# Kernel tuning notes

Hardware: AMD Instinct MI355X
Metric: run time of the kernel (lower is better)

## Reference

```python
import jax, jax.numpy as jnp
import numpy as np

B, T, DM, H = 4, 2048, 1024, 16
D = DM // H  # head_dim = 64


def setup_inputs() -> dict:
    key = jax.random.key(0)
    ks = jax.random.split(key, 10)
    s = 0.02
    return {
        "query": jax.random.normal(ks[0], (B, T, DM), jnp.float32),
        "key": jax.random.normal(ks[1], (B, T, DM), jnp.float32),
        "value": jax.random.normal(ks[2], (B, T, DM), jnp.float32),
        "Wq": jax.random.normal(ks[3], (DM, DM), jnp.float32) * s,
        "bq": jnp.zeros((DM,), jnp.float32),
        "Wk": jax.random.normal(ks[4], (DM, DM), jnp.float32) * s,
        "bk": jnp.zeros((DM,), jnp.float32),
        "Wv": jax.random.normal(ks[5], (DM, DM), jnp.float32) * s,
        "bv": jnp.zeros((DM,), jnp.float32),
        "Wo": jax.random.normal(ks[6], (DM, DM), jnp.float32) * s,
        "bo": jnp.zeros((DM,), jnp.float32),
        "gate_w": jax.random.normal(ks[7], (H, D, D), jnp.float32) * s,
        "gate_b": jax.random.normal(ks[8], (H, D), jnp.float32),
    }


def _split_heads(x):
    # (B, T, DM) -> (B, H, T, D)
    b, t, _ = x.shape
    return x.reshape(b, t, H, D).transpose(0, 2, 1, 3)


def reference(query, key, value, Wq, bq, Wk, bk, Wv, bv, Wo, bo, gate_w, gate_b):
    q = _split_heads(query @ Wq + bq)   # (B,H,T,D)
    k = _split_heads(key @ Wk + bk)
    v = _split_heads(value @ Wv + bv)
    scale = 1.0 / jnp.sqrt(jnp.asarray(D, q.dtype))
    scores = jnp.einsum("bhqd,bhkd->bhqk", q, k) * scale  # (B,H,Tq,Tk)
    attn = jax.nn.softmax(scores, axis=-1)
    y = jnp.einsum("bhqk,bhkd->bhqd", attn, v)            # (B,H,T,D)
    # per-head elementwise gating: sigmoid(W_h y + b_h)
    gate = jax.nn.sigmoid(jnp.einsum("bhtd,hde->bhte", y, gate_w) + gate_b[None, :, None, :])
    y = y * gate
    y = y.transpose(0, 2, 1, 3).reshape(y.shape[0], y.shape[2], H * D)  # merge heads
    return y @ Wo + bo
```

## Files before the change

kernel.cpp:

```cpp
#include <hip/hip_runtime.h>
#include <stdint.h>

typedef unsigned short u16;
typedef uint32_t u32;
typedef __attribute__((ext_vector_type(8))) short bf16x8;
typedef __attribute__((ext_vector_type(4))) float f32x4;
typedef __attribute__((ext_vector_type(4))) u32 u32x4;

__device__ __forceinline__ u16 f2b(float x) {
  union { float f; uint32_t u; } v; v.f = x;
  uint32_t u = v.u;
  return (u16)((u + 0x7fffu + ((u >> 16) & 1u)) >> 16);
}

__device__ __forceinline__ float fexp2(float x) {
  float r;
  asm("v_exp_f32 %0, %1" : "=v"(r) : "v"(x));
  return r;
}

__device__ __forceinline__ u32 cvtpk(float lo, float hi) {
  u32 r;
  asm("v_cvt_pk_bf16_f32 %0, %1, %2" : "=v"(r) : "v"(lo), "v"(hi));
  return r;
}

__device__ __forceinline__ void gload_lds16(const void* g, void* l) {
  __builtin_amdgcn_global_load_lds(
      (const __attribute__((address_space(1))) void*)g,
      (__attribute__((address_space(3))) void*)l, 16, 0, 0);
}

__global__ __launch_bounds__(256) void cvt3_f32_bf16(const float* __restrict__ q,
                                                     const float* __restrict__ k,
                                                     const float* __restrict__ v,
                                                     u16* __restrict__ xq,
                                                     u16* __restrict__ xk,
                                                     u16* __restrict__ xv, int n4) {
  int idx = blockIdx.x * 256 + threadIdx.x;
  if (idx >= n4) return;
  const int z = blockIdx.y;
  const float* in = z == 0 ? q : z == 1 ? k : v;
  u16* out = z == 0 ? xq : z == 1 ? xk : xv;
  float4 vv = ((const float4*)in)[idx];
  ushort4 o;
  o.x = f2b(vv.x); o.y = f2b(vv.y); o.z = f2b(vv.z); o.w = f2b(vv.w);
  ((ushort4*)out)[idx] = o;
}

__global__ __launch_bounds__(256) void transpose_cvt4(const float* __restrict__ w0,
                                                      const float* __restrict__ w1,
                                                      const float* __restrict__ w2,
                                                      const float* __restrict__ w3,
                                                      u16* __restrict__ o0,
                                                      u16* __restrict__ o1,
                                                      u16* __restrict__ o2,
                                                      u16* __restrict__ o3) {
  __shared__ float t[64][65];
  const int z = blockIdx.z;
  const float* inp = z == 0 ? w0 : z == 1 ? w1 : z == 2 ? w2 : w3;
  u16* outp = z == 0 ? o0 : z == 1 ? o1 : z == 2 ? o2 : o3;
  int r0 = blockIdx.x * 64, c0 = blockIdx.y * 64;
  for (int i = 0; i < 16; ++i) {
    int idx = i * 256 + threadIdx.x;
    int r = idx >> 6, c = idx & 63;
    t[r][c] = inp[(size_t)(r0 + r) * 1024 + (c0 + c)];
  }
  __syncthreads();
  for (int i = 0; i < 16; ++i) {
    int idx = i * 256 + threadIdx.x;
    int c = idx >> 6, r = idx & 63;
    outp[(size_t)(c0 + c) * 1024 + (r0 + r)] = f2b(t[r][c]);
  }
}

__global__ __launch_bounds__(256) void transpose_gate(const float* __restrict__ in,
                                                      u16* __restrict__ out) {
  __shared__ float t[64][65];
  const float* inp = in + (size_t)blockIdx.z * 4096;
  u16* outp = out + (size_t)blockIdx.z * 4096;
  for (int i = 0; i < 16; ++i) {
    int idx = i * 256 + threadIdx.x;
    int r = idx >> 6, c = idx & 63;
    t[r][c] = inp[(size_t)r * 64 + c];
  }
  __syncthreads();
  for (int i = 0; i < 16; ++i) {
    int idx = i * 256 + threadIdx.x;
    int c = idx >> 6, r = idx & 63;
    outp[(size_t)c * 64 + r] = f2b(t[r][c]);
  }
}

template <int MODE>
__device__ __forceinline__ void gemm_body(const u16* __restrict__ A,
                                          const u16* __restrict__ Bt,
                                          const float* __restrict__ bias,
                                          void* __restrict__ Cout,
                                          int M, int N, int K, float scale,
                                          u16* lA, u16* lB, int bm, int bn) {
  const int tid = threadIdx.x;
  const int wave = tid >> 6, lane = tid & 63;
  const int l15 = lane & 15, l4 = lane >> 4;
  const int wr = (wave >> 1) * 64, wc = (wave & 1) * 64;
  f32x4 acc[4][4];
  for (int a = 0; a < 4; ++a)
    for (int b = 0; b < 4; ++b)
      for (int j = 0; j < 4; ++j) acc[a][b][j] = 0.f;
  const u16* Ab = A + (size_t)bm * 128 * K;
  const u16* Bb = Bt + (size_t)bn * 128 * K;
  for (int kt = 0; kt < K; kt += 64) {
    __syncthreads();
#pragma unroll
    for (int i = 0; i < 4; ++i) {
      int p = i * 256 + tid;
      int r = p >> 3, kc = p & 7, skc = kc ^ (r & 7);
      gload_lds16(Ab + (size_t)r * K + kt + skc * 8, &lA[p * 8]);
    }
#pragma unroll
    for (int i = 0; i < 4; ++i) {
      int p = i * 256 + tid;
      int r = p >> 3, kc = p & 7, skc = kc ^ (r & 7);
      gload_lds16(Bb + (size_t)r * K + kt + skc * 8, &lB[p * 8]);
    }
    __syncthreads();
#pragma unroll
    for (int kk = 0; kk < 2; ++kk) {
      const int kch = kk * 4 + l4;
      bf16x8 af[4], bfr[4];
#pragma unroll
      for (int mt = 0; mt < 4; ++mt) {
        int r = wr + mt * 16 + l15;
        af[mt] = *(const bf16x8*)&lA[r * 64 + ((kch ^ (r & 7)) << 3)];
      }
#pragma unroll
      for (int nt = 0; nt < 4; ++nt) {
        int r = wc + nt * 16 + l15;
        bfr[nt] = *(const bf16x8*)&lB[r * 64 + ((kch ^ (r & 7)) << 3)];
      }
      __builtin_amdgcn_s_setprio(1);
#pragma unroll
      for (int mt = 0; mt < 4; ++mt)
#pragma unroll
        for (int nt = 0; nt < 4; ++nt)
          acc[mt][nt] = __builtin_amdgcn_mfma_f32_16x16x32_bf16(af[mt], bfr[nt],
                                                                acc[mt][nt], 0, 0, 0);
      __builtin_amdgcn_s_setprio(0);
    }
  }
  float bval[4];
  float bvalm[4][4];
  if constexpr (MODE == 2) {
#pragma unroll
    for (int mt = 0; mt < 4; ++mt)
#pragma unroll
      for (int i = 0; i < 4; ++i)
        bvalm[mt][i] = bias[bm * 128 + wr + mt * 16 + l4 * 4 + i];
  } else {
#pragma unroll
    for (int nt = 0; nt < 4; ++nt) bval[nt] = bias[bn * 128 + wc + nt * 16 + l15];
  }
#pragma unroll
  for (int mt = 0; mt < 4; ++mt) {
#pragma unroll
    for (int nt = 0; nt < 4; ++nt) {
      int n = bn * 128 + wc + nt * 16 + l15;
#pragma unroll
      for (int i = 0; i < 4; ++i) {
        int m = bm * 128 + wr + mt * 16 + l4 * 4 + i;
        if constexpr (MODE == 0) {
          ((float*)Cout)[(size_t)m * N + n] = acc[mt][nt][i] + bval[nt];
        } else if constexpr (MODE == 1) {
          float v = acc[mt][nt][i] + bval[nt];
          int bb = m >> 11, t = m & 2047, hh = n >> 6, d = n & 63;
          ((u16*)Cout)[(((size_t)bb * 16 + hh) * 2048 + t) * 64 + d] = f2b(v * scale);
        } else {
          float v = acc[mt][nt][i] + bvalm[mt][i];
          int bb = n >> 11, t = n & 2047, hh = m >> 6, d = m & 63;
          ((u16*)Cout)[(((size_t)bb * 16 + hh) * 64 + d) * 2048 + t] = f2b(v);
        }
      }
    }
  }
}

__device__ __forceinline__ void gemm_swizzle(int& i64, int& i8) {
  int lid = blockIdx.x + (blockIdx.y << 6);
  int xcd = lid & 7, s = lid >> 3;
  i64 = xcd * 8 + (s & 7);
  i8 = s >> 3;
}

__global__ __launch_bounds__(256) void gemm_qkv(const u16* __restrict__ Xq,
                                                const u16* __restrict__ Xk,
                                                const u16* __restrict__ Xv,
                                                const u16* __restrict__ WqT,
                                                const u16* __restrict__ WkT,
                                                const u16* __restrict__ WvT,
                                                const float* __restrict__ bq,
                                                const float* __restrict__ bk,
                                                const float* __restrict__ bv,
                                                u16* __restrict__ Qb,
                                                u16* __restrict__ Kb,
                                                u16* __restrict__ Vtr, float qscale) {
  __shared__ __align__(16) u16 lA[128 * 64];
  __shared__ __align__(16) u16 lB[128 * 64];
  const int z = blockIdx.z;
  int i64, i8;
  gemm_swizzle(i64, i8);
  if (z == 2) {
    gemm_body<2>(WvT, Xv, bv, Vtr, 1024, 8192, 1024, 1.0f, lA, lB, i8, i64);
  } else {
    const u16* A = z == 0 ? Xq : Xk;
    const u16* Bt = z == 0 ? WqT : WkT;
    const float* bias = z == 0 ? bq : bk;
    u16* C = z == 0 ? Qb : Kb;
    float scale = z == 0 ? qscale : 1.0f;
    gemm_body<1>(A, Bt, bias, C, 8192, 1024, 1024, scale, lA, lB, i64, i8);
  }
}

__global__ __launch_bounds__(256) void gemm_out(const u16* __restrict__ A,
                                                const u16* __restrict__ Bt,
                                                const float* __restrict__ bias,
                                                float* __restrict__ C) {
  __shared__ __align__(16) u16 lA[128 * 64];
  __shared__ __align__(16) u16 lB[128 * 64];
  int i64, i8;
  gemm_swizzle(i64, i8);
  gemm_body<0>(A, Bt, bias, C, 8192, 1024, 1024, 1.0f, lA, lB, i64, i8);
}

__global__ __launch_bounds__(256) void attn_fused(const u16* __restrict__ Qb,
                                                  const u16* __restrict__ Kb,
                                                  const u16* __restrict__ Vt,
                                                  const u16* __restrict__ GwT,
                                                  const float* __restrict__ gate_b,
                                                  u16* __restrict__ Yg) {
  __shared__ __align__(16) u16 lds[16384];
  const int tid = threadIdx.x;
  const int w = tid >> 6, lane = tid & 63;
  const int l15 = lane & 15, l4 = lane >> 4;
  const int bid = blockIdx.x;
  const int xcd = bid & 7, slot = bid >> 3;
  const int bh = xcd * 8 + (slot >> 4);
  const int qt = slot & 15;
  const int b = bh >> 4, h = bh & 15;

  const u16* QgA = Qb + ((size_t)bh * 2048 + qt * 128 + w * 32 + l15) * 64;
  const u16* QgB = QgA + 16 * 64;
  bf16x8 qA0 = *(const bf16x8*)(QgA + l4 * 8);
  bf16x8 qA1 = *(const bf16x8*)(QgA + 32 + l4 * 8);
  bf16x8 qB0 = *(const bf16x8*)(QgB + l4 * 8);
  bf16x8 qB1 = *(const bf16x8*)(QgB + 32 + l4 * 8);

  const bf16x8 ones = {0x3F80, 0x3F80, 0x3F80, 0x3F80, 0x3F80, 0x3F80, 0x3F80, 0x3F80};
  const f32x4 fz = {0.f, 0.f, 0.f, 0.f};

  f32x4 accA[4], accB[4], lsA, lsB;
#pragma unroll
  for (int nt = 0; nt < 4; ++nt)
#pragma unroll
    for (int j = 0; j < 4; ++j) { accA[nt][j] = 0.f; accB[nt][j] = 0.f; }
#pragma unroll
  for (int j = 0; j < 4; ++j) { lsA[j] = 0.f; lsB[j] = 0.f; }

  const u16* f0 = lds + l15 * 64 + ((l4 ^ (l15 & 7)) << 3);
  const u16* f1 = lds + l15 * 64 + (((4 + l4) ^ (l15 & 7)) << 3);

  const int r0 = tid >> 3, kc0 = tid & 7, skc = kc0 ^ (r0 & 7);
  const int sr = ((r0 << 1) & 0x38) | ((r0 >> 3) & 4) | (r0 & 3);
  const u16* kp  = Kb + (size_t)bh * 131072 + (size_t)sr * 64 + skc * 8;
  const u16* kp2 = kp + 256;
  const u16* vp  = Vt + (size_t)bh * 131072 + (size_t)r0 * 2048 + skc * 8;
  const u16* vp2 = vp + (size_t)32 * 2048;
  u16* dK = lds + tid * 8;
  u16* dV = lds + 8192 + tid * 8;

#define STAGE(c)                                                     \
  do {                                                               \
    gload_lds16(kp, dK + (c)*4096);                                  \
    gload_lds16(kp2, dK + (c)*4096 + 2048);                          \
    gload_lds16(vp, dV + (c)*4096);                                  \
    gload_lds16(vp2, dV + (c)*4096 + 2048);                          \
    kp += 4096; kp2 += 4096; vp += 64; vp2 += 64;                    \
  } while (0)

#define COMPUTE(c)                                                            \
  do {                                                                        \
    bf16x8 kf0[4], kf1[4];                                                    \
    _Pragma("unroll") for (int nt = 0; nt < 4; ++nt) {                        \
      kf0[nt] = *(const bf16x8*)(f0 + (c)*4096 + nt * 1024);                  \
      kf1[nt] = *(const bf16x8*)(f1 + (c)*4096 + nt * 1024);                  \
    }                                                                         \
    f32x4 sA[4], sB[4];                                                       \
    __builtin_amdgcn_s_setprio(1);                                            \
    _Pragma("unroll") for (int nt = 0; nt < 4; ++nt) {                        \
      sA[nt] = __builtin_amdgcn_mfma_f32_16x16x32_bf16(kf0[nt], qA0, fz, 0, 0, 0); \
      sA[nt] = __builtin_amdgcn_mfma_f32_16x16x32_bf16(kf1[nt], qA1, sA[nt], 0, 0, 0); \
      sB[nt] = __builtin_amdgcn_mfma_f32_16x16x32_bf16(kf0[nt], qB0, fz, 0, 0, 0); \
      sB[nt] = __builtin_amdgcn_mfma_f32_16x16x32_bf16(kf1[nt], qB1, sB[nt], 0, 0, 0); \
    }                                                                         \
    __builtin_amdgcn_s_setprio(0);                                            \
    union { u32x4 u; bf16x8 bv; } a0, a1, b0, b1;                             \
    a0.u[0] = cvtpk(fexp2(sA[0][0]), fexp2(sA[0][1]));                        \
    a0.u[1] = cvtpk(fexp2(sA[0][2]), fexp2(sA[0][3]));                        \
    a0.u[2] = cvtpk(fexp2(sA[2][0]), fexp2(sA[2][1]));                        \
    a0.u[3] = cvtpk(fexp2(sA[2][2]), fexp2(sA[2][3]));                        \
    a1.u[0] = cvtpk(fexp2(sA[1][0]), fexp2(sA[1][1]));                        \
    a1.u[1] = cvtpk(fexp2(sA[1][2]), fexp2(sA[1][3]));                        \
    a1.u[2] = cvtpk(fexp2(sA[3][0]), fexp2(sA[3][1]));                        \
    a1.u[3] = cvtpk(fexp2(sA[3][2]), fexp2(sA[3][3]));                        \
    b0.u[0] = cvtpk(fexp2(sB[0][0]), fexp2(sB[0][1]));                        \
    b0.u[1] = cvtpk(fexp2(sB[0][2]), fexp2(sB[0][3]));                        \
    b0.u[2] = cvtpk(fexp2(sB[2][0]), fexp2(sB[2][1]));                        \
    b0.u[3] = cvtpk(fexp2(sB[2][2]), fexp2(sB[2][3]));                        \
    b1.u[0] = cvtpk(fexp2(sB[1][0]), fexp2(sB[1][1]));                        \
    b1.u[1] = cvtpk(fexp2(sB[1][2]), fexp2(sB[1][3]));                        \
    b1.u[2] = cvtpk(fexp2(sB[3][0]), fexp2(sB[3][1]));                        \
    b1.u[3] = cvtpk(fexp2(sB[3][2]), fexp2(sB[3][3]));                        \
    __builtin_amdgcn_s_setprio(1);                                            \
    lsA = __builtin_amdgcn_mfma_f32_16x16x32_bf16(ones, a0.bv, lsA, 0, 0, 0); \
    lsA = __builtin_amdgcn_mfma_f32_16x16x32_bf16(ones, a1.bv, lsA, 0, 0, 0); \
    lsB = __builtin_amdgcn_mfma_f32_16x16x32_bf16(ones, b0.bv, lsB, 0, 0, 0); \
    lsB = __builtin_amdgcn_mfma_f32_16x16x32_bf16(ones, b1.bv, lsB, 0, 0, 0); \
    bf16x8 vf0[4], vf1[4];                                                    \
    _Pragma("unroll") for (int nt = 0; nt < 4; ++nt) {                        \
      vf0[nt] = *(const bf16x8*)(f0 + 8192 + (c)*4096 + nt * 1024);           \
      vf1[nt] = *(const bf16x8*)(f1 + 8192 + (c)*4096 + nt * 1024);           \
    }                                                                         \
    _Pragma("unroll") for (int nt = 0; nt < 4; ++nt) {                        \
      accA[nt] = __builtin_amdgcn_mfma_f32_16x16x32_bf16(vf0[nt], a0.bv, accA[nt], 0, 0, 0); \
      accA[nt] = __builtin_amdgcn_mfma_f32_16x16x32_bf16(vf1[nt], a1.bv, accA[nt], 0, 0, 0); \
      accB[nt] = __builtin_amdgcn_mfma_f32_16x16x32_bf16(vf0[nt], b0.bv, accB[nt], 0, 0, 0); \
      accB[nt] = __builtin_amdgcn_mfma_f32_16x16x32_bf16(vf1[nt], b1.bv, accB[nt], 0, 0, 0); \
    }                                                                         \
    __builtin_amdgcn_s_setprio(0);                                            \
  } while (0)

  STAGE(0);
  __syncthreads();
  for (int it = 0; it < 16; ++it) {
    STAGE(1);
    COMPUTE(0);
    __syncthreads();
    if (it < 15) STAGE(0);
    COMPUTE(1);
    __syncthreads();
  }
#undef STAGE
#undef COMPUTE

  bf16x8 gwf[2][4];
  {
    const u16* g = GwT + (size_t)h * 4096;
#pragma unroll
    for (int kk = 0; kk < 2; ++kk)
#pragma unroll
      for (int et = 0; et < 4; ++et)
        gwf[kk][et] = *(const bf16x8*)(g + (et * 16 + l15) * 64 + (kk * 4 + l4) * 8);
  }
  const float* gb = gate_b + h * 64;
  const int rsw = (l15 & 7) << 2;

#define EPILOGUE(accX, lsX, g)                                                 \
  do {                                                                         \
    float inv = 1.f / lsX[0];                                                  \
    float y[4][4];                                                             \
    _Pragma("unroll") for (int nt = 0; nt < 4; ++nt)                           \
      _Pragma("unroll") for (int i = 0; i < 4; ++i) y[nt][i] = accX[nt][i] * inv; \
    u32* ws32 = (u32*)lds + w * 2048 + (g)*1024;                               \
    _Pragma("unroll") for (int nt = 0; nt < 4; ++nt) {                         \
      u32 y0 = cvtpk(y[nt][0], y[nt][1]);                                      \
      u32 y1 = cvtpk(y[nt][2], y[nt][3]);                                      \
      int col = (nt * 8 + l4 * 2) ^ rsw;                                       \
      *(uint64_t*)(ws32 + l15 * 64 + col) = ((uint64_t)y1 << 32) | y0;         \
    }                                                                          \
    asm volatile("s_waitcnt lgkmcnt(0)" ::: "memory");                         \
    bf16x8 yf[2];                                                              \
    yf[0] = *(const bf16x8*)(ws32 + l15 * 64 + ((l4 * 4) ^ rsw));              \
    yf[1] = *(const bf16x8*)(ws32 + l15 * 64 + ((16 + l4 * 4) ^ rsw));         \
    f32x4 g4[4];                                                               \
    _Pragma("unroll") for (int et = 0; et < 4; ++et)                           \
      _Pragma("unroll") for (int j = 0; j < 4; ++j) g4[et][j] = 0.f;           \
    _Pragma("unroll") for (int kk = 0; kk < 2; ++kk)                           \
      _Pragma("unroll") for (int et = 0; et < 4; ++et)                         \
        g4[et] = __builtin_amdgcn_mfma_f32_16x16x32_bf16(gwf[kk][et], yf[kk], g4[et], 0, 0, 0); \
    u32 ok[4][2];                                                              \
    _Pragma("unroll") for (int et = 0; et < 4; ++et) {                         \
      float o[4];                                                              \
      _Pragma("unroll") for (int i = 0; i < 4; ++i) {                          \
        float gv = g4[et][i] + gb[et * 16 + l4 * 4 + i];                       \
        float sg = 1.f / (1.f + __expf(-gv));                                  \
        o[i] = y[et][i] * sg;                                                  \
      }                                                                        \
      ok[et][0] = cvtpk(o[0], o[1]);                                           \
      ok[et][1] = cvtpk(o[2], o[3]);                                           \
    }                                                                          \
    asm volatile("s_waitcnt lgkmcnt(0)" ::: "memory");                         \
    _Pragma("unroll") for (int et = 0; et < 4; ++et) {                         \
      int col = (et * 8 + l4 * 2) ^ rsw;                                       \
      *(uint64_t*)(ws32 + l15 * 64 + col) = ((uint64_t)ok[et][1] << 32) | ok[et][0]; \
    }                                                                          \
    asm volatile("s_waitcnt lgkmcnt(0)" ::: "memory");                         \
    {                                                                          \
      int rr = lane >> 2, c = lane & 3;                                        \
      int rs2 = (rr & 7) << 2;                                                 \
      u32x4 d0 = *(const u32x4*)(ws32 + rr * 64 + ((c * 4) ^ rs2));            \
      u32x4 d1 = *(const u32x4*)(ws32 + rr * 64 + (((c + 4) * 4) ^ rs2));      \
      size_t row = (size_t)b * 2048 + qt * 128 + w * 32 + (g)*16 + rr;         \
      u32* og = (u32*)(Yg + row * 1024 + h * 64);                              \
      *(u32x4*)(og + c * 4) = d0;                                              \
      *(u32x4*)(og + (c + 4) * 4) = d1;                                        \
    }                                                                          \
  } while (0)

  EPILOGUE(accA, lsA, 0);
  EPILOGUE(accB, lsB, 1);
#undef EPILOGUE
}

extern "C" void kernel_launch(void* const* d_in, const int* in_sizes, int n_in,
                              void* d_out, int out_size, void* d_ws, size_t ws_size,
                              hipStream_t stream) {
  (void)in_sizes; (void)n_in; (void)out_size; (void)ws_size;
  const float* query  = (const float*)d_in[0];
  const float* key    = (const float*)d_in[1];
  const float* value  = (const float*)d_in[2];
  const float* Wq     = (const float*)d_in[3];
  const float* bq     = (const float*)d_in[4];
  const float* Wk     = (const float*)d_in[5];
  const float* bk     = (const float*)d_in[6];
  const float* Wv     = (const float*)d_in[7];
  const float* bv     = (const float*)d_in[8];
  const float* Wo     = (const float*)d_in[9];
  const float* bo     = (const float*)d_in[10];
  const float* gate_w = (const float*)d_in[11];
  const float* gate_b = (const float*)d_in[12];

  const size_t XN = (size_t)8192 * 1024;
  const size_t WN = (size_t)1024 * 1024;
  char* ws = (char*)d_ws;
  size_t off = 0;
  auto nxt = [&](size_t bytes) {
    char* p = ws + off;
    off += (bytes + 255) & ~(size_t)255;
    return p;
  };
  u16* Xq  = (u16*)nxt(XN * 2);
  u16* Xk  = (u16*)nxt(XN * 2);
  u16* Xv  = (u16*)nxt(XN * 2);
  u16* WqT = (u16*)nxt(WN * 2);
  u16* WkT = (u16*)nxt(WN * 2);
  u16* WvT = (u16*)nxt(WN * 2);
  u16* WoT = (u16*)nxt(WN * 2);
  u16* GwT = (u16*)nxt((size_t)16 * 64 * 64 * 2);
  u16* Qb  = (u16*)nxt(XN * 2);
  u16* Kb  = (u16*)nxt(XN * 2);
  u16* Vtr = (u16*)nxt(XN * 2);
  u16* Yg  = (u16*)nxt(XN * 2);

  int n4 = (int)(XN / 4);
  cvt3_f32_bf16<<<dim3(n4 / 256, 3), 256, 0, stream>>>(query, key, value, Xq, Xk, Xv, n4);
  transpose_cvt4<<<dim3(16, 16, 4), 256, 0, stream>>>(Wq, Wk, Wv, Wo, WqT, WkT, WvT, WoT);
  transpose_gate<<<dim3(1, 1, 16), 256, 0, stream>>>(gate_w, GwT);

  gemm_qkv<<<dim3(64, 8, 3), 256, 0, stream>>>(Xq, Xk, Xv, WqT, WkT, WvT, bq, bk, bv,
                                               Qb, Kb, Vtr, 0.125f * 1.44269504f);
  attn_fused<<<1024, 256, 0, stream>>>(Qb, Kb, Vtr, GwT, gate_b, Yg);
  gemm_out<<<dim3(64, 8), 256, 0, stream>>>(Yg, WoT, bo, (float*)d_out);
}
```

Before: 206.7 us.

## Software-pipeline attention loop with triple-buffered K/V and skewed QK/PV stages

The fused attention loop is restructured into a three-stage software pipeline. The exp/convert work for one KV chunk overlaps the PV MFMAs of the previous chunk and the QK^T MFMAs of the next chunk, and K/V staging in LDS moves from two buffers to three. The aim is to hide the transcendental latency and the global-to-LDS loads behind matrix work, replacing __syncthreads with an explicit vmcnt wait plus barrier. In exchange it uses more LDS (48 KB) and keeps score and probability registers live across stages, which may cut occupancy.

```diff
diff --git a/kernel.cpp b/kernel.cpp
--- a/kernel.cpp
+++ b/kernel.cpp
@@ -237,7 +237,7 @@
                                                   const u16* __restrict__ GwT,
                                                   const float* __restrict__ gate_b,
                                                   u16* __restrict__ Yg) {
-  __shared__ __align__(16) u16 lds[16384];
+  __shared__ __align__(16) u16 lds[24576];
   const int tid = threadIdx.x;
   const int w = tid >> 6, lane = tid & 63;
   const int l15 = lane & 15, l4 = lane >> 4;
@@ -265,6 +265,9 @@
 #pragma unroll
   for (int j = 0; j < 4; ++j) { lsA[j] = 0.f; lsB[j] = 0.f; }
 
+  f32x4 sA[4], sB[4];
+  bf16x8 pA0, pA1, pB0, pB1;
+
   const u16* f0 = lds + l15 * 64 + ((l4 ^ (l15 & 7)) << 3);
   const u16* f1 = lds + l15 * 64 + (((4 + l4) ^ (l15 & 7)) << 3);
 
@@ -275,7 +278,7 @@
   const u16* vp  = Vt + (size_t)bh * 131072 + (size_t)r0 * 2048 + skc * 8;
   const u16* vp2 = vp + (size_t)32 * 2048;
   u16* dK = lds + tid * 8;
-  u16* dV = lds + 8192 + tid * 8;
+  u16* dV = lds + 12288 + tid * 8;
 
 #define STAGE(c)                                                     \
   do {                                                               \
@@ -286,14 +289,13 @@
     kp += 4096; kp2 += 4096; vp += 64; vp2 += 64;                    \
   } while (0)
 
-#define COMPUTE(c)                                                            \
+#define QKT(c)                                                                \
   do {                                                                        \
     bf16x8 kf0[4], kf1[4];                                                    \
     _Pragma("unroll") for (int nt = 0; nt < 4; ++nt) {                        \
       kf0[nt] = *(const bf16x8*)(f0 + (c)*4096 + nt * 1024);                  \
       kf1[nt] = *(const bf16x8*)(f1 + (c)*4096 + nt * 1024);                  \
     }                                                                         \
-    f32x4 sA[4], sB[4];                                                       \
     __builtin_amdgcn_s_setprio(1);                                            \
     _Pragma("unroll") for (int nt = 0; nt < 4; ++nt) {                        \
       sA[nt] = __builtin_amdgcn_mfma_f32_16x16x32_bf16(kf0[nt], qA0, fz, 0, 0, 0); \
@@ -302,6 +304,10 @@
       sB[nt] = __builtin_amdgcn_mfma_f32_16x16x32_bf16(kf1[nt], qB1, sB[nt], 0, 0, 0); \
     }                                                                         \
     __builtin_amdgcn_s_setprio(0);                                            \
+  } while (0)
+
+#define EXPP()                                                                \
+  do {                                                                        \
     union { u32x4 u; bf16x8 bv; } a0, a1, b0, b1;                             \
     a0.u[0] = cvtpk(fexp2(sA[0][0]), fexp2(sA[0][1]));                        \
     a0.u[1] = cvtpk(fexp2(sA[0][2]), fexp2(sA[0][3]));                        \
@@ -319,37 +325,62 @@
     b1.u[1] = cvtpk(fexp2(sB[1][2]), fexp2(sB[1][3]));                        \
     b1.u[2] = cvtpk(fexp2(sB[3][0]), fexp2(sB[3][1]));                        \
     b1.u[3] = cvtpk(fexp2(sB[3][2]), fexp2(sB[3][3]));                        \
-    __builtin_amdgcn_s_setprio(1);                                            \
-    lsA = __builtin_amdgcn_mfma_f32_16x16x32_bf16(ones, a0.bv, lsA, 0, 0, 0); \
-    lsA = __builtin_amdgcn_mfma_f32_16x16x32_bf16(ones, a1.bv, lsA, 0, 0, 0); \
-    lsB = __builtin_amdgcn_mfma_f32_16x16x32_bf16(ones, b0.bv, lsB, 0, 0, 0); \
-    lsB = __builtin_amdgcn_mfma_f32_16x16x32_bf16(ones, b1.bv, lsB, 0, 0, 0); \
+    pA0 = a0.bv; pA1 = a1.bv; pB0 = b0.bv; pB1 = b1.bv;                       \
+  } while (0)
+
+#define PVC(c)                                                                \
+  do {                                                                        \
     bf16x8 vf0[4], vf1[4];                                                    \
     _Pragma("unroll") for (int nt = 0; nt < 4; ++nt) {                        \
-      vf0[nt] = *(const bf16x8*)(f0 + 8192 + (c)*4096 + nt * 1024);           \
-      vf1[nt] = *(const bf16x8*)(f1 + 8192 + (c)*4096 + nt * 1024);           \
+      vf0[nt] = *(const bf16x8*)(f0 + 12288 + (c)*4096 + nt * 1024);          \
+      vf1[nt] = *(const bf16x8*)(f1 + 12288 + (c)*4096 + nt * 1024);          \
     }                                                                         \
+    __builtin_amdgcn_s_setprio(1);                                            \
+    lsA = __builtin_amdgcn_mfma_f32_16x16x32_bf16(ones, pA0, lsA, 0, 0, 0);   \
+    lsA = __builtin_amdgcn_mfma_f32_16x16x32_bf16(ones, pA1, lsA, 0, 0, 0);   \
+    lsB = __builtin_amdgcn_mfma_f32_16x16x32_bf16(ones, pB0, lsB, 0, 0, 0);   \
+    lsB = __builtin_amdgcn_mfma_f32_16x16x32_bf16(ones, pB1, lsB, 0, 0, 0);   \
     _Pragma("unroll") for (int nt = 0; nt < 4; ++nt) {                        \
-      accA[nt] = __builtin_amdgcn_mfma_f32_16x16x32_bf16(vf0[nt], a0.bv, accA[nt], 0, 0, 0); \
-      accA[nt] = __builtin_amdgcn_mfma_f32_16x16x32_bf16(vf1[nt], a1.bv, accA[nt], 0, 0, 0); \
-      accB[nt] = __builtin_amdgcn_mfma_f32_16x16x32_bf16(vf0[nt], b0.bv, accB[nt], 0, 0, 0); \
-      accB[nt] = __builtin_amdgcn_mfma_f32_16x16x32_bf16(vf1[nt], b1.bv, accB[nt], 0, 0, 0); \
+      accA[nt] = __builtin_amdgcn_mfma_f32_16x16x32_bf16(vf0[nt], pA0, accA[nt], 0, 0, 0); \
+      accA[nt] = __builtin_amdgcn_mfma_f32_16x16x32_bf16(vf1[nt], pA1, accA[nt], 0, 0, 0); \
+      accB[nt] = __builtin_amdgcn_mfma_f32_16x16x32_bf16(vf0[nt], pB0, accB[nt], 0, 0, 0); \
+      accB[nt] = __builtin_amdgcn_mfma_f32_16x16x32_bf16(vf1[nt], pB1, accB[nt], 0, 0, 0); \
     }                                                                         \
     __builtin_amdgcn_s_setprio(0);                                            \
   } while (0)
 
+#define VBAR()                                        \
+  do {                                                \
+    asm volatile("s_waitcnt vmcnt(0)" ::: "memory");  \
+    __builtin_amdgcn_s_barrier();                     \
+  } while (0)
+
+#define ITER(cp, cn) \
+  do { STAGE(cn); PVC(cp); EXPP(); VBAR(); QKT(cn); } while (0)
+
   STAGE(0);
+  VBAR();
+  QKT(0);
+  STAGE(1);
+  EXPP();
+  VBAR();
+  QKT(1);
+
+  for (int it = 0; it < 10; ++it) {
+    ITER(0, 2);
+    ITER(1, 0);
+    ITER(2, 1);
+  }
+  PVC(0);
+  EXPP();
+  PVC(1);
   __syncthreads();
-  for (int it = 0; it < 16; ++it) {
-    STAGE(1);
-    COMPUTE(0);
-    __syncthreads();
-    if (it < 15) STAGE(0);
-    COMPUTE(1);
-    __syncthreads();
-  }
 #undef STAGE
-#undef COMPUTE
+#undef QKT
+#undef EXPP
+#undef PVC
+#undef VBAR
+#undef ITER
 
   bf16x8 gwf[2][4];
   {
```

After: 203.7 us. About the same (-1.4%).

## Use 256x128 GEMM tiles with 512 threads and triple-buffered async LDS loads

Applied to the files above, without the earlier changes.

Replaces the 128x128, 256-thread GEMM body with a 256x128 tile run by 8 waves. Global-to-LDS loads are triple-buffered so the next two K-steps are in flight during compute, with vmcnt waits and one barrier per step instead of two syncthreads. Source and fragment addresses are precomputed, and the block-to-tile mapping is changed to spread tiles across XCDs. The cost is 144KB of LDS per block and a grid that shrinks to 256 blocks per GEMM, which may limit occupancy.

```diff
diff --git a/kernel.cpp b/kernel.cpp
--- a/kernel.cpp
+++ b/kernel.cpp
@@ -93,61 +93,101 @@
 }
 
 template <int MODE>
-__device__ __forceinline__ void gemm_body(const u16* __restrict__ A,
-                                          const u16* __restrict__ Bt,
-                                          const float* __restrict__ bias,
-                                          void* __restrict__ Cout,
-                                          int M, int N, int K, float scale,
-                                          u16* lA, u16* lB, int bm, int bn) {
+__device__ __forceinline__ void gemm256_body(const u16* __restrict__ A,
+                                             const u16* __restrict__ Bt,
+                                             const float* __restrict__ bias,
+                                             void* __restrict__ Cout,
+                                             int M, int N, int K, float scale,
+                                             u16* lds, int bm, int bn) {
   const int tid = threadIdx.x;
-  const int wave = tid >> 6, lane = tid & 63;
+  const int w = tid >> 6, lane = tid & 63;
   const int l15 = lane & 15, l4 = lane >> 4;
-  const int wr = (wave >> 1) * 64, wc = (wave & 1) * 64;
+  const int wm = w & 3, wn = w >> 2;
+  const int wr = wm * 64, wc = wn * 64;
+
   f32x4 acc[4][4];
+#pragma unroll
   for (int a = 0; a < 4; ++a)
+#pragma unroll
     for (int b = 0; b < 4; ++b)
+#pragma unroll
       for (int j = 0; j < 4; ++j) acc[a][b][j] = 0.f;
-  const u16* Ab = A + (size_t)bm * 128 * K;
+
+  const u16* Ab = A + (size_t)bm * 256 * K;
   const u16* Bb = Bt + (size_t)bn * 128 * K;
-  for (int kt = 0; kt < K; kt += 64) {
-    __syncthreads();
-#pragma unroll
-    for (int i = 0; i < 4; ++i) {
-      int p = i * 256 + tid;
-      int r = p >> 3, kc = p & 7, skc = kc ^ (r & 7);
-      gload_lds16(Ab + (size_t)r * K + kt + skc * 8, &lA[p * 8]);
-    }
-#pragma unroll
-    for (int i = 0; i < 4; ++i) {
-      int p = i * 256 + tid;
-      int r = p >> 3, kc = p & 7, skc = kc ^ (r & 7);
-      gload_lds16(Bb + (size_t)r * K + kt + skc * 8, &lB[p * 8]);
-    }
-    __syncthreads();
+
+  const u16* aS[4];
+  u16* aD[4];
+  const u16* bS[2];
+  u16* bD[2];
+#pragma unroll
+  for (int i = 0; i < 4; ++i) {
+    int p = i * 512 + tid;
+    int r = p >> 3, kc = p & 7, skc = kc ^ (r & 7);
+    aS[i] = Ab + (size_t)r * K + skc * 8;
+    aD[i] = lds + p * 8;
+  }
+#pragma unroll
+  for (int j = 0; j < 2; ++j) {
+    int p = j * 512 + tid;
+    int r = p >> 3, kc = p & 7, skc = kc ^ (r & 7);
+    bS[j] = Bb + (size_t)r * K + skc * 8;
+    bD[j] = lds + 16384 + p * 8;
+  }
+
+  const int xr = l15 & 7;
+  const u16* fA0 = lds + (wr + l15) * 64 + ((l4 ^ xr) << 3);
+  const u16* fA1 = lds + (wr + l15) * 64 + (((4 + l4) ^ xr) << 3);
+  const u16* fB0 = lds + 16384 + (wc + l15) * 64 + ((l4 ^ xr) << 3);
+  const u16* fB1 = lds + 16384 + (wc + l15) * 64 + (((4 + l4) ^ xr) << 3);
+
+  auto GSTAGE = [&](int buf, int t) {
+#pragma unroll
+    for (int i = 0; i < 4; ++i) gload_lds16(aS[i] + t * 64, aD[i] + buf * 24576);
+#pragma unroll
+    for (int j = 0; j < 2; ++j) gload_lds16(bS[j] + t * 64, bD[j] + buf * 24576);
+  };
+  auto GCOMP = [&](int buf) {
+    const int o = buf * 24576;
 #pragma unroll
     for (int kk = 0; kk < 2; ++kk) {
-      const int kch = kk * 4 + l4;
-      bf16x8 af[4], bfr[4];
-#pragma unroll
-      for (int mt = 0; mt < 4; ++mt) {
-        int r = wr + mt * 16 + l15;
-        af[mt] = *(const bf16x8*)&lA[r * 64 + ((kch ^ (r & 7)) << 3)];
-      }
-#pragma unroll
-      for (int nt = 0; nt < 4; ++nt) {
-        int r = wc + nt * 16 + l15;
-        bfr[nt] = *(const bf16x8*)&lB[r * 64 + ((kch ^ (r & 7)) << 3)];
-      }
+      bf16x8 af[4], bf[4];
+#pragma unroll
+      for (int mt = 0; mt < 4; ++mt)
+        af[mt] = *(const bf16x8*)((kk ? fA1 : fA0) + o + mt * 1024);
+#pragma unroll
+      for (int nt = 0; nt < 4; ++nt)
+        bf[nt] = *(const bf16x8*)((kk ? fB1 : fB0) + o + nt * 1024);
       __builtin_amdgcn_s_setprio(1);
 #pragma unroll
       for (int mt = 0; mt < 4; ++mt)
 #pragma unroll
         for (int nt = 0; nt < 4; ++nt)
-          acc[mt][nt] = __builtin_amdgcn_mfma_f32_16x16x32_bf16(af[mt], bfr[nt],
+          acc[mt][nt] = __builtin_amdgcn_mfma_f32_16x16x32_bf16(af[mt], bf[nt],
                                                                 acc[mt][nt], 0, 0, 0);
       __builtin_amdgcn_s_setprio(0);
     }
-  }
+  };
+
+  GSTAGE(0, 0);
+  GSTAGE(1, 1);
+  asm volatile("s_waitcnt vmcnt(6)" ::: "memory");
+  __builtin_amdgcn_s_barrier();
+
+#pragma unroll
+  for (int t = 0; t < 16; ++t) {
+    const int buf = t % 3;
+    if (t < 14) GSTAGE((t + 2) % 3, t + 2);
+    GCOMP(buf);
+    if (t < 15) {
+      if (t < 14)
+        asm volatile("s_waitcnt vmcnt(6)" ::: "memory");
+      else
+        asm volatile("s_waitcnt vmcnt(0)" ::: "memory");
+      __builtin_amdgcn_s_barrier();
+    }
+  }
+
   float bval[4];
   float bvalm[4][4];
   if constexpr (MODE == 2) {
@@ -155,7 +195,7 @@
     for (int mt = 0; mt < 4; ++mt)
 #pragma unroll
       for (int i = 0; i < 4; ++i)
-        bvalm[mt][i] = bias[bm * 128 + wr + mt * 16 + l4 * 4 + i];
+        bvalm[mt][i] = bias[bm * 256 + wr + mt * 16 + l4 * 4 + i];
   } else {
 #pragma unroll
     for (int nt = 0; nt < 4; ++nt) bval[nt] = bias[bn * 128 + wc + nt * 16 + l15];
@@ -167,68 +207,58 @@
       int n = bn * 128 + wc + nt * 16 + l15;
 #pragma unroll
       for (int i = 0; i < 4; ++i) {
-        int m = bm * 128 + wr + mt * 16 + l4 * 4 + i;
+        int m = bm * 256 + wr + mt * 16 + l4 * 4 + i;
         if constexpr (MODE == 0) {
           ((float*)Cout)[(size_t)m * N + n] = acc[mt][nt][i] + bval[nt];
         } else if constexpr (MODE == 1) {
           float v = acc[mt][nt][i] + bval[nt];
-          int bb = m >> 11, t = m & 2047, hh = n >> 6, d = n & 63;
-          ((u16*)Cout)[(((size_t)bb * 16 + hh) * 2048 + t) * 64 + d] = f2b(v * scale);
+          int bb = m >> 11, t2 = m & 2047, hh = n >> 6, d = n & 63;
+          ((u16*)Cout)[(((size_t)bb * 16 + hh) * 2048 + t2) * 64 + d] = f2b(v * scale);
         } else {
           float v = acc[mt][nt][i] + bvalm[mt][i];
-          int bb = n >> 11, t = n & 2047, hh = m >> 6, d = m & 63;
-          ((u16*)Cout)[(((size_t)bb * 16 + hh) * 64 + d) * 2048 + t] = f2b(v);
+          int bb = n >> 11, t2 = n & 2047, hh = m >> 6, d = m & 63;
+          ((u16*)Cout)[(((size_t)bb * 16 + hh) * 64 + d) * 2048 + t2] = f2b(v);
         }
       }
     }
   }
 }
 
-__device__ __forceinline__ void gemm_swizzle(int& i64, int& i8) {
-  int lid = blockIdx.x + (blockIdx.y << 6);
-  int xcd = lid & 7, s = lid >> 3;
-  i64 = xcd * 8 + (s & 7);
-  i8 = s >> 3;
-}
-
-__global__ __launch_bounds__(256) void gemm_qkv(const u16* __restrict__ Xq,
-                                                const u16* __restrict__ Xk,
-                                                const u16* __restrict__ Xv,
-                                                const u16* __restrict__ WqT,
-                                                const u16* __restrict__ WkT,
-                                                const u16* __restrict__ WvT,
-                                                const float* __restrict__ bq,
-                                                const float* __restrict__ bk,
-                                                const float* __restrict__ bv,
-                                                u16* __restrict__ Qb,
-                                                u16* __restrict__ Kb,
-                                                u16* __restrict__ Vtr, float qscale) {
-  __shared__ __align__(16) u16 lA[128 * 64];
-  __shared__ __align__(16) u16 lB[128 * 64];
-  const int z = blockIdx.z;
-  int i64, i8;
-  gemm_swizzle(i64, i8);
+__global__ __launch_bounds__(512, 2) void gemm_qkv256(const u16* __restrict__ Xq,
+                                                      const u16* __restrict__ Xk,
+                                                      const u16* __restrict__ Xv,
+                                                      const u16* __restrict__ WqT,
+                                                      const u16* __restrict__ WkT,
+                                                      const u16* __restrict__ WvT,
+                                                      const float* __restrict__ bq,
+                                                      const float* __restrict__ bk,
+                                                      const float* __restrict__ bv,
+                                                      u16* __restrict__ Qb,
+                                                      u16* __restrict__ Kb,
+                                                      u16* __restrict__ Vtr,
+                                                      float qscale) {
+  __shared__ __align__(16) u16 lds[73728];
+  const int z = blockIdx.y;
+  const int lid = blockIdx.x;
+  const int xcd = lid & 7, s = lid >> 3;
   if (z == 2) {
-    gemm_body<2>(WvT, Xv, bv, Vtr, 1024, 8192, 1024, 1.0f, lA, lB, i8, i64);
+    int bm = s & 3, bn = (s >> 2) * 8 + xcd;
+    gemm256_body<2>(WvT, Xv, bv, Vtr, 1024, 8192, 1024, 1.0f, lds, bm, bn);
+  } else if (z == 0) {
+    gemm256_body<1>(Xq, WqT, bq, Qb, 8192, 1024, 1024, qscale, lds, s, xcd);
   } else {
-    const u16* A = z == 0 ? Xq : Xk;
-    const u16* Bt = z == 0 ? WqT : WkT;
-    const float* bias = z == 0 ? bq : bk;
-    u16* C = z == 0 ? Qb : Kb;
-    float scale = z == 0 ? qscale : 1.0f;
-    gemm_body<1>(A, Bt, bias, C, 8192, 1024, 1024, scale, lA, lB, i64, i8);
-  }
-}
-
-__global__ __launch_bounds__(256) void gemm_out(const u16* __restrict__ A,
-                                                const u16* __restrict__ Bt,
-                                                const float* __restrict__ bias,
-                                                float* __restrict__ C) {
-  __shared__ __align__(16) u16 lA[128 * 64];
-  __shared__ __align__(16) u16 lB[128 * 64];
-  int i64, i8;
-  gemm_swizzle(i64, i8);
-  gemm_body<0>(A, Bt, bias, C, 8192, 1024, 1024, 1.0f, lA, lB, i64, i8);
+    gemm256_body<1>(Xk, WkT, bk, Kb, 8192, 1024, 1024, 1.0f, lds, s, xcd);
+  }
+}
+
+__global__ __launch_bounds__(512, 2) void gemm_out256(const u16* __restrict__ A,
+                                                      const u16* __restrict__ Bt,
+                                                      const float* __restrict__ bias,
+                                                      float* __restrict__ C) {
+  __shared__ __align__(16) u16 lds[73728];
+  const int lid = blockIdx.x;
+  const int xcd = lid & 7, s = lid >> 3;
+  gemm256_body<0>(A, Bt, bias, C, 8192, 1024, 1024, 1.0f, lds, s, xcd);
 }
 
 __global__ __launch_bounds__(256) void attn_fused(const u16* __restrict__ Qb,
@@ -465,8 +495,9 @@
   transpose_cvt4<<<dim3(16, 16, 4), 256, 0, stream>>>(Wq, Wk, Wv, Wo, WqT, WkT, WvT, WoT);
   transpose_gate<<<dim3(1, 1, 16), 256, 0, stream>>>(gate_w, GwT);
 
-  gemm_qkv<<<dim3(64, 8, 3), 256, 0, stream>>>(Xq, Xk, Xv, WqT, WkT, WvT, bq, bk, bv,
-                                               Qb, Kb, Vtr, 0.125f * 1.44269504f);
+  gemm_qkv256<<<dim3(256, 3), 512, 0, stream>>>(Xq, Xk, Xv, WqT, WkT, WvT,
+                                                bq, bk, bv, Qb, Kb, Vtr,
+                                                0.125f * 1.44269504f);
   attn_fused<<<1024, 256, 0, stream>>>(Qb, Kb, Vtr, GwT, gate_b, Yg);
-  gemm_out<<<dim3(64, 8), 256, 0, stream>>>(Yg, WoT, bo, (float*)d_out);
-}
+  gemm_out256<<<256, 512, 0, stream>>>(Yg, WoT, bo, (float*)d_out);
+}
```

Result: no change. 207.2 us (+0.2%).
